# Kernel optimization log

Measured on AMD Instinct MI355X. Metric: run time of the kernel, lower is better.

Reference implementation:

```python
import jax, jax.numpy as jnp
import numpy as np

N = 50000   # nodes
E = 1600000 # edges
G = 512     # graphs in batch
IN_DIM, EMBED, H, D = 64, 128, 4, 32
D1, D2, D3 = 128, 64, 16
NEG_SLOPE = 0.2  # DGL GATConv default


def setup_inputs() -> dict:
    key = jax.random.key(0)
    ks = jax.random.split(key, 16)
    def glorot(k, shape):
        fan = shape[0] + shape[-1]
        return jax.random.normal(k, shape, jnp.float32) * jnp.sqrt(2.0 / fan)
    return {
        "feature": jax.random.normal(ks[0], (N, IN_DIM), jnp.float32),
        "src": jax.random.randint(ks[1], (E,), 0, N, jnp.int32),
        "dst": jax.random.randint(ks[2], (E,), 0, N, jnp.int32),
        "graph_ids": jnp.sort(jax.random.randint(ks[3], (N,), 0, G, jnp.int32)),
        "W0": glorot(ks[4], (IN_DIM, EMBED)), "b0": jnp.zeros((EMBED,), jnp.float32),
        "Wfc": glorot(ks[5], (EMBED, H * D)),
        "attn_l": glorot(ks[6], (H, D)), "attn_r": glorot(ks[7], (H, D)),
        "gat_bias": jnp.zeros((H * D,), jnp.float32),
        "W1": glorot(ks[8], (H * D, D1)), "b1": jnp.zeros((D1,), jnp.float32),
        "W2": glorot(ks[9], (D1, D2)), "b2": jnp.zeros((D2,), jnp.float32),
        "W3": glorot(ks[10], (D2, D3)), "b3": jnp.zeros((D3,), jnp.float32),
    }


def reference(feature, src, dst, graph_ids, W0, b0, Wfc, attn_l, attn_r,
              gat_bias, W1, b1, W2, b2, W3, b3):
    # initial dense embed
    h = feature @ W0 + b0                                   # [N, EMBED]
    # GATConv
    feat = (h @ Wfc).reshape(N, H, D)                       # [N,H,D]
    el = jnp.einsum('nhd,hd->nh', feat, attn_l)             # [N,H]
    er = jnp.einsum('nhd,hd->nh', feat, attn_r)
    e = jax.nn.leaky_relu(el[src] + er[dst], NEG_SLOPE)     # [E,H]
    # segment softmax over incoming edges of each dst node
    m = jax.ops.segment_max(e, dst, num_segments=N)         # [N,H]
    ex = jnp.exp(e - m[dst])                                # [E,H]
    denom = jax.ops.segment_sum(ex, dst, num_segments=N)    # [N,H]
    a = ex / denom[dst]                                     # [E,H]
    msg = a[:, :, None] * feat[src]                         # [E,H,D]
    rst = jax.ops.segment_sum(msg, dst, num_segments=N)     # [N,H,D]
    rst = rst + gat_bias.reshape(1, H, D)
    hn = rst.reshape(N, H * D)
    # AvgPooling per graph
    sums = jax.ops.segment_sum(hn, graph_ids, num_segments=G)           # [G,H*D]
    cnts = jax.ops.segment_sum(jnp.ones((N,), hn.dtype), graph_ids, num_segments=G)
    hg = sums / jnp.maximum(cnts, 1.0)[:, None]
    # dense head
    out = jax.nn.elu(hg)
    out = jax.nn.elu(out @ W1 + b1)
    out = jax.nn.elu(out @ W2 + b2)
    out = out @ W3 + b3                                     # [G, D3]
    atten = a[:, :, None]                                   # [E,H,1] like DGL
    return out, atten
```

## Files before the change

kernel.cpp:

```cpp
#include <hip/hip_runtime.h>
#include <hip/hip_fp16.h>
#include <math.h>

#define N_NODES 50000
#define E_EDGES 1600000
#define G_GRAPHS 512
#define IN_DIM 64
#define EMBED 128
#define HD 128
#define NHEAD 4
#define D1 128
#define D2 64
#define D3 16
#define NEG_SLOPE 0.2f
#define NB ((N_NODES + 127) >> 7)
#define HT_TILE 4096
#define HT_BLOCKS ((E_EDGES + HT_TILE - 1) / HT_TILE)
#define PT_TILE 8192
#define PT_BLOCKS ((E_EDGES + PT_TILE - 1) / PT_TILE)
#define K1_TILES ((N_NODES + 63) / 64)
#define FB_CAP 8192
#define M2_EDGE_BLK ((E_EDGES + 2047) / 2048)

typedef float vfloat4 __attribute__((ext_vector_type(4)));
typedef float vfloat2 __attribute__((ext_vector_type(2)));
typedef unsigned short ushort_t;

static __device__ __forceinline__ float leaky(float x) { return x > 0.f ? x : NEG_SLOPE * x; }

__global__ void __launch_bounds__(256) k0hg(const int* __restrict__ dst, int* __restrict__ ghist,
                                            const float* __restrict__ W0, const float* __restrict__ b0,
                                            const float* __restrict__ Wfc, float* __restrict__ Wc,
                                            float* __restrict__ bc) {
    __shared__ int lh[NB];
    const int t = threadIdx.x;
    if (blockIdx.x < HT_BLOCKS) {
        for (int i = t; i < NB; i += 256) lh[i] = 0;
        __syncthreads();
        const long e0 = (long)blockIdx.x * HT_TILE;
#pragma unroll
        for (int k = 0; k < HT_TILE / 256; ++k) {
            long e = e0 + t + k * 256;
            if (e < E_EDGES) atomicAdd(&lh[dst[e] >> 7], 1);
        }
        __syncthreads();
        for (int i = t; i < NB; i += 256) {
            int v = lh[i];
            if (v) atomicAdd(&ghist[i], v);
        }
    } else {
        int tid = (int)(blockIdx.x - HT_BLOCKS) * 256 + t;
        if (tid < IN_DIM * HD) {
            int i = tid >> 7, j = tid & 127;
            float acc = 0.f;
            for (int k = 0; k < EMBED; ++k) acc += W0[i * EMBED + k] * Wfc[k * HD + j];
            Wc[tid] = acc;
        } else if (tid < IN_DIM * HD + HD) {
            int j = tid - IN_DIM * HD;
            float acc = 0.f;
            for (int k = 0; k < EMBED; ++k) acc += b0[k] * Wfc[k * HD + j];
            bc[j] = acc;
        }
    }
}

#define SMEM_BYTES 53248
__global__ void __launch_bounds__(256) k1pt(
    const float* __restrict__ A, const float* __restrict__ W,
    const float* __restrict__ b, const float* __restrict__ attn_l,
    const float* __restrict__ attn_r,
    const int* __restrict__ src, const int* __restrict__ dst,
    const int* __restrict__ ghist, int* __restrict__ cursor0,
    unsigned char* __restrict__ feat, float* __restrict__ el,
    float* __restrict__ er, unsigned int* __restrict__ part) {
    __shared__ __align__(16) char smem[SMEM_BYTES];
    const int t = threadIdx.x;
    if (blockIdx.x < K1_TILES) {
        float* Ws = (float*)smem;
        float(*As)[68] = (float(*)[68])(smem + 32768);
        const int cc = t & 31, rt = t >> 5;
        const int c0 = cc * 4, r0 = rt * 8;
        const int row0 = (int)blockIdx.x * 64;
        {
            const float4* Wg = (const float4*)W;
            float4* Wl = (float4*)Ws;
#pragma unroll
            for (int j = 0; j < (IN_DIM * HD / 4) / 256; ++j) Wl[t + j * 256] = Wg[t + j * 256];
        }
#pragma unroll
        for (int j = 0; j < 4; ++j) {
            int i2 = t + j * 256;
            int row = i2 >> 4, kq = i2 & 15;
            int gr = row0 + row;
            float4 v = (gr < N_NODES) ? *(const float4*)(A + (size_t)gr * IN_DIM + kq * 4)
                                      : make_float4(0.f, 0.f, 0.f, 0.f);
            *(float4*)&As[row][kq * 4] = v;
        }
        __syncthreads();
        float acc[8][4];
#pragma unroll
        for (int i = 0; i < 8; ++i)
#pragma unroll
            for (int j = 0; j < 4; ++j) acc[i][j] = 0.f;
        for (int k4 = 0; k4 < IN_DIM / 4; ++k4) {
            vfloat4 w0 = *(const vfloat4*)&Ws[(k4 * 4 + 0) * HD + c0];
            vfloat4 w1 = *(const vfloat4*)&Ws[(k4 * 4 + 1) * HD + c0];
            vfloat4 w2 = *(const vfloat4*)&Ws[(k4 * 4 + 2) * HD + c0];
            vfloat4 w3 = *(const vfloat4*)&Ws[(k4 * 4 + 3) * HD + c0];
#pragma unroll
            for (int i = 0; i < 8; ++i) {
                vfloat4 a = *(const vfloat4*)&As[r0 + i][k4 * 4];
#pragma unroll
                for (int j = 0; j < 4; ++j)
                    acc[i][j] += a.x * w0[j] + a.y * w1[j] + a.z * w2[j] + a.w * w3[j];
            }
        }
        {
            vfloat4 bcv = *(const vfloat4*)(b + c0);
#pragma unroll
            for (int i = 0; i < 8; ++i)
#pragma unroll
                for (int j = 0; j < 4; ++j) acc[i][j] += bcv[j];
        }
#pragma unroll
        for (int i = 0; i < 8; ++i) {
            int gr = row0 + r0 + i;
            if (gr < N_NODES) {
                unsigned int ww = __builtin_amdgcn_cvt_pk_fp8_f32(acc[i][0], acc[i][1], 0, false);
                ww = __builtin_amdgcn_cvt_pk_fp8_f32(acc[i][2], acc[i][3], ww, true);
                *(unsigned int*)(feat + (size_t)gr * HD + c0) = ww;
            }
        }
        {
            vfloat4 al = *(const vfloat4*)(attn_l + c0);
            vfloat4 ar = *(const vfloat4*)(attn_r + c0);
            float pl[8], pr[8];
#pragma unroll
            for (int i = 0; i < 8; ++i) {
                pl[i] = acc[i][0] * al[0] + acc[i][1] * al[1] + acc[i][2] * al[2] + acc[i][3] * al[3];
                pr[i] = acc[i][0] * ar[0] + acc[i][1] * ar[1] + acc[i][2] * ar[2] + acc[i][3] * ar[3];
            }
#pragma unroll
            for (int off = 1; off <= 4; off <<= 1) {
#pragma unroll
                for (int i = 0; i < 8; ++i) {
                    pl[i] += __shfl_xor(pl[i], off);
                    pr[i] += __shfl_xor(pr[i], off);
                }
            }
            if ((cc & 7) == 0) {
                const int h = cc >> 3;
#pragma unroll
                for (int i = 0; i < 8; ++i) {
                    int gr = row0 + r0 + i;
                    if (gr < N_NODES) {
                        el[gr * 4 + h] = pl[i];
                        er[gr * 4 + h] = pr[i];
                    }
                }
            }
        }
    } else {
        int(*hist)[NB] = (int(*)[NB])smem;
        int(*lcur)[NB] = (int(*)[NB])(smem + 6256);
        int* tot = (int*)(smem + 12512);
        int* offs = (int*)(smem + 14076);
        int* base_s = (int*)(smem + 15640);
        int* gt = (int*)(smem + 17204);
        int* offsG = (int*)(smem + 18768);
        unsigned int* stage = (unsigned int*)(smem + 20336);
        const int lane = t & 63, wid = t >> 6;
        const int tile = (int)blockIdx.x - K1_TILES;
        const long e0 = (long)tile * PT_TILE;
        const int cnt = (int)min((long)PT_TILE, (long)E_EDGES - e0);
        for (int i = t; i < NB; i += 256) {
            hist[0][i] = 0; hist[1][i] = 0; hist[2][i] = 0; hist[3][i] = 0;
            gt[i] = ghist[i];
        }
        __syncthreads();
        unsigned int v[PT_TILE / 256];
#pragma unroll
        for (int k = 0; k < PT_TILE / 256; ++k) {
            int i = t + k * 256;
            if (i < cnt) {
                int d = dst[e0 + i];
                v[k] = ((unsigned int)d << 16) | (unsigned int)src[e0 + i];
                atomicAdd(&hist[wid][d >> 7], 1);
            } else v[k] = 0xFFFFFFFFu;
        }
        __syncthreads();
        for (int i = t; i < NB; i += 256) {
            int h0 = hist[0][i], h1 = hist[1][i], h2 = hist[2][i], h3 = hist[3][i];
            hist[0][i] = 0; hist[1][i] = h0; hist[2][i] = h0 + h1; hist[3][i] = h0 + h1 + h2;
            tot[i] = h0 + h1 + h2 + h3;
        }
        __syncthreads();
        if (wid == 0) {
            int run = 0;
            for (int c = 0; c < (NB + 63) / 64; ++c) {
                int i = c * 64 + lane;
                int vv = (i < NB) ? tot[i] : 0;
                int incl = vv;
#pragma unroll
                for (int off = 1; off < 64; off <<= 1) {
                    int o = __shfl_up(incl, off, 64);
                    if (lane >= off) incl += o;
                }
                if (i < NB) offs[i] = run + incl - vv;
                run += __shfl(incl, 63, 64);
            }
        } else if (wid == 1) {
            int run = 0;
            for (int c = 0; c < (NB + 63) / 64; ++c) {
                int i = c * 64 + lane;
                int vv = (i < NB) ? gt[i] : 0;
                int incl = vv;
#pragma unroll
                for (int off = 1; off < 64; off <<= 1) {
                    int o = __shfl_up(incl, off, 64);
                    if (lane >= off) incl += o;
                }
                if (i < NB) offsG[i] = run + incl - vv;
                run += __shfl(incl, 63, 64);
            }
        }
        __syncthreads();
        for (int i = t; i < NB; i += 256) {
            int tt2 = tot[i];
            base_s[i] = offsG[i] + (tt2 ? atomicAdd(&cursor0[i], tt2) : 0);
            int ob = offs[i];
            lcur[0][i] = ob + hist[0][i];
            lcur[1][i] = ob + hist[1][i];
            lcur[2][i] = ob + hist[2][i];
            lcur[3][i] = ob + hist[3][i];
        }
        __syncthreads();
#pragma unroll
        for (int k = 0; k < PT_TILE / 256; ++k) {
            if (v[k] != 0xFFFFFFFFu) {
                int bb = v[k] >> 23;
                int pos = atomicAdd(&lcur[wid][bb], 1);
                stage[pos] = v[k];
            }
        }
        __syncthreads();
        for (int i = t; i < cnt; i += 256) {
            unsigned int p = stage[i];
            int bb = p >> 23;
            part[base_s[bb] + (i - offs[bb])] = p & 0x7FFFFFu;
        }
    }
}

__global__ void __launch_bounds__(256) fb_fill(const unsigned int* __restrict__ part,
                                               const int* __restrict__ ghist,
                                               int* __restrict__ rowstart,
                                               ushort_t* __restrict__ csr_src) {
    const int b = blockIdx.x, t = threadIdx.x, lane = t & 63, wid = t >> 6;
    __shared__ int degl[4][128], totl[128], offl[128], curl[4][128];
    __shared__ int red[4], s0s[2];
    __shared__ ushort_t lsrc[FB_CAP];
    {
        int partial = 0;
        for (int i = t; i < b; i += 256) partial += ghist[i];
#pragma unroll
        for (int off = 32; off; off >>= 1) partial += __shfl_xor(partial, off);
        if (lane == 0) red[wid] = partial;
        if (t < 128) { degl[0][t] = 0; degl[1][t] = 0; degl[2][t] = 0; degl[3][t] = 0; }
        __syncthreads();
        if (t == 0) {
            int s0 = red[0] + red[1] + red[2] + red[3];
            s0s[0] = s0;
            s0s[1] = s0 + ghist[b];
        }
        __syncthreads();
    }
    const int s0 = s0s[0], s1 = s0s[1];
    const int cnt = s1 - s0;
    for (int i = t; i < cnt; i += 256) {
        unsigned int p = part[s0 + i];
        atomicAdd(&degl[wid][p >> 16], 1);
    }
    __syncthreads();
    if (t < 128) {
        int d0 = degl[0][t], d1 = degl[1][t], d2 = degl[2][t], d3 = degl[3][t];
        degl[0][t] = 0; degl[1][t] = d0; degl[2][t] = d0 + d1; degl[3][t] = d0 + d1 + d2;
        totl[t] = d0 + d1 + d2 + d3;
    }
    __syncthreads();
    if (wid == 0) {
        int run = 0;
        for (int c = 0; c < 2; ++c) {
            int i = c * 64 + lane;
            int vv = totl[i];
            int incl = vv;
#pragma unroll
            for (int off = 1; off < 64; off <<= 1) {
                int o = __shfl_up(incl, off, 64);
                if (lane >= off) incl += o;
            }
            offl[i] = run + incl - vv;
            run += __shfl(incl, 63, 64);
        }
    }
    __syncthreads();
    if (t < 128) {
        int ob = offl[t];
        curl[0][t] = ob + degl[0][t];
        curl[1][t] = ob + degl[1][t];
        curl[2][t] = ob + degl[2][t];
        curl[3][t] = ob + degl[3][t];
        int node = (b << 7) + t;
        if (node < N_NODES) rowstart[node] = s0 + ob;
    }
    if (b == 0 && t == 0) rowstart[N_NODES] = E_EDGES;
    __syncthreads();
    if (cnt <= FB_CAP) {
        for (int i = t; i < cnt; i += 256) {
            unsigned int p = part[s0 + i];
            int pos = atomicAdd(&curl[wid][p >> 16], 1);
            lsrc[pos] = (ushort_t)(p & 0xFFFFu);
        }
        __syncthreads();
        for (int i = t; i < cnt; i += 256) csr_src[s0 + i] = lsrc[i];
    } else {
        for (int i = t; i < cnt; i += 256) {
            unsigned int p = part[s0 + i];
            int pos = atomicAdd(&curl[wid][p >> 16], 1);
            csr_src[s0 + pos] = (ushort_t)(p & 0xFFFFu);
        }
    }
}

__global__ void __launch_bounds__(256) k6_aggregate(
    const ushort_t* __restrict__ csr_src, const int* __restrict__ rowstart,
    const float* __restrict__ el, const float* __restrict__ er,
    const unsigned char* __restrict__ feat, const float* __restrict__ gat_bias,
    float* __restrict__ er_rd, float* __restrict__ hn) {
    __shared__ uint2 s_pk[4][64][4];
    const int wid = threadIdx.x >> 6;
    const int lane = threadIdx.x & 63;
    const int n = blockIdx.x * 4 + wid;
    if (n >= N_NODES) return;
    const int start = rowstart[n];
    const int end = rowstart[n + 1];
    const int deg = end - start;

    const int e0 = lane >> 2;
    const int h = lane & 3;
    const float erh = er[n * 4 + h];
    float sm = 0.f;
    for (int base = 0; base < deg; base += 16) {
        const int e = base + e0;
        if (e < deg) {
            const int s = csr_src[start + e];
            const float ex = __expf(leaky(el[s * 4 + h] + erh));
            sm += ex;
            if (e < 64)
                s_pk[wid][e][h] = make_uint2((unsigned int)s << 7, __float_as_uint(ex));
        }
    }
#pragma unroll
    for (int off = 4; off <= 32; off <<= 1) sm += __shfl_xor(sm, off);
    const float rd = sm > 0.f ? 1.f / sm : 0.f;
    if (lane < 4) {
        er_rd[(size_t)n * 8 + lane] = erh;
        er_rd[(size_t)n * 8 + 4 + lane] = rd;
    }

    const int g4 = lane >> 4, gl = lane & 15;
    const int h2 = gl >> 2;
    const float rdh = __shfl(rd, h2);
    vfloat2 acc0 = {0.f, 0.f}, acc1 = {0.f, 0.f}, acc2 = {0.f, 0.f}, acc3 = {0.f, 0.f};

    if (deg <= 64) {
        const uint2* pk = &s_pk[wid][0][h2];
        const unsigned char* fg = feat + (gl << 3);
        int idx = g4;
        for (; idx + 4 < deg; idx += 8) {
            const uint2 pA = pk[idx * 4];
            const uint2 pB = pk[(idx + 4) * 4];
            const uint2 wA = *(const uint2*)(fg + pA.x);
            const uint2 wB = *(const uint2*)(fg + pB.x);
            const float exA = __uint_as_float(pA.y);
            const float exB = __uint_as_float(pB.y);
            const vfloat2 eA = {exA, exA}, eB = {exB, exB};
            acc0 += eA * __builtin_amdgcn_cvt_pk_f32_fp8(wA.x, false);
            acc1 += eA * __builtin_amdgcn_cvt_pk_f32_fp8(wA.x, true);
            acc2 += eA * __builtin_amdgcn_cvt_pk_f32_fp8(wA.y, false);
            acc3 += eA * __builtin_amdgcn_cvt_pk_f32_fp8(wA.y, true);
            acc0 += eB * __builtin_amdgcn_cvt_pk_f32_fp8(wB.x, false);
            acc1 += eB * __builtin_amdgcn_cvt_pk_f32_fp8(wB.x, true);
            acc2 += eB * __builtin_amdgcn_cvt_pk_f32_fp8(wB.y, false);
            acc3 += eB * __builtin_amdgcn_cvt_pk_f32_fp8(wB.y, true);
        }
        if (idx < deg) {
            const uint2 p = pk[idx * 4];
            const uint2 w = *(const uint2*)(fg + p.x);
            const float ex = __uint_as_float(p.y);
            const vfloat2 ev = {ex, ex};
            acc0 += ev * __builtin_amdgcn_cvt_pk_f32_fp8(w.x, false);
            acc1 += ev * __builtin_amdgcn_cvt_pk_f32_fp8(w.x, true);
            acc2 += ev * __builtin_amdgcn_cvt_pk_f32_fp8(w.y, false);
            acc3 += ev * __builtin_amdgcn_cvt_pk_f32_fp8(w.y, true);
        }
    } else {
        const float erh2 = __shfl(erh, h2);
        const unsigned char* fg = feat + (gl << 3);
        for (int e = start + g4; e < end; e += 4) {
            const unsigned int s = csr_src[e];
            const float ex = __expf(leaky(el[s * 4 + h2] + erh2));
            const vfloat2 ev = {ex, ex};
            const uint2 w = *(const uint2*)(fg + ((size_t)s << 7));
            acc0 += ev * __builtin_amdgcn_cvt_pk_f32_fp8(w.x, false);
            acc1 += ev * __builtin_amdgcn_cvt_pk_f32_fp8(w.x, true);
            acc2 += ev * __builtin_amdgcn_cvt_pk_f32_fp8(w.y, false);
            acc3 += ev * __builtin_amdgcn_cvt_pk_f32_fp8(w.y, true);
        }
    }
    {
        const vfloat2 rv = {rdh, rdh};
        acc0 *= rv; acc1 *= rv; acc2 *= rv; acc3 *= rv;
    }
#pragma unroll
    for (int off = 16; off <= 32; off <<= 1) {
        acc0.x += __shfl_xor(acc0.x, off);
        acc0.y += __shfl_xor(acc0.y, off);
        acc1.x += __shfl_xor(acc1.x, off);
        acc1.y += __shfl_xor(acc1.y, off);
        acc2.x += __shfl_xor(acc2.x, off);
        acc2.y += __shfl_xor(acc2.y, off);
        acc3.x += __shfl_xor(acc3.x, off);
        acc3.y += __shfl_xor(acc3.y, off);
    }
    if (lane < 16) {
        const float4 b0 = ((const float4*)gat_bias)[gl * 2];
        const float4 b1 = ((const float4*)gat_bias)[gl * 2 + 1];
        float4* hp = (float4*)(hn + (size_t)n * HD + gl * 8);
        hp[0] = make_float4(acc0.x + b0.x, acc0.y + b0.y, acc1.x + b0.z, acc1.y + b0.w);
        hp[1] = make_float4(acc2.x + b1.x, acc2.y + b1.y, acc3.x + b1.z, acc3.y + b1.w);
    }
}

__global__ void __launch_bounds__(512) m2b_mlp_attn(
    const int* __restrict__ src, const int* __restrict__ dst,
    const float* __restrict__ el, const float* __restrict__ er_rd,
    const float* __restrict__ hn, const int* __restrict__ graph_ids,
    const float* __restrict__ W1, const float* __restrict__ b1,
    const float* __restrict__ W2, const float* __restrict__ b2,
    const float* __restrict__ W3, const float* __restrict__ b3,
    float* __restrict__ a_out, float* __restrict__ out) {
    const int t = threadIdx.x;
    if (blockIdx.x < G_GRAPHS) {
        const int g = (int)blockIdx.x;
        const int tt = t & 127, part = t >> 7;
        __shared__ int bounds[2];
        __shared__ double pool[4][128];
        __shared__ double x[128], y[128];
        if (t < 2) {
            const int target = g + t;
            int lo = 0, hi = N_NODES;
            while (lo < hi) {
                int mid = (lo + hi) >> 1;
                if (graph_ids[mid] < target) lo = mid + 1; else hi = mid;
            }
            bounds[t] = lo;
        }
        __syncthreads();
        const int lo = bounds[0], hi = bounds[1];
        double s = 0.0;
        for (int n = lo + part; n < hi; n += 4) s += (double)hn[(size_t)n * HD + tt];
        pool[part][tt] = s;
        __syncthreads();
        if (t < 128) {
            const double cnt = (double)(hi - lo);
            const double sum = pool[0][t] + pool[1][t] + pool[2][t] + pool[3][t];
            const double v = sum / fmax(cnt, 1.0);
            x[t] = v > 0.0 ? v : expm1(v);
        }
        __syncthreads();
        if (t < 128) {
            double acc = (double)b1[t];
            for (int k = 0; k < HD; ++k) acc += x[k] * (double)W1[k * D1 + t];
            y[t] = acc > 0.0 ? acc : expm1(acc);
        }
        __syncthreads();
        if (t < D2) {
            double a2 = (double)b2[t];
            for (int k = 0; k < D1; ++k) a2 += y[k] * (double)W2[k * D2 + t];
            x[t] = a2 > 0.0 ? a2 : expm1(a2);
        }
        __syncthreads();
        if (t < D3) {
            double a3 = (double)b3[t];
            for (int k = 0; k < D2; ++k) a3 += x[k] * (double)W3[k * D3 + t];
            out[g * D3 + t] = (float)a3;
        }
    } else {
        const long base = (long)(blockIdx.x - G_GRAPHS) * 2048 + t;
        bool ok[4];
        int sx[4], dx[4];
#pragma unroll
        for (int k = 0; k < 4; ++k) {
            const long e = base + (long)k * 512;
            ok[k] = e < E_EDGES;
            const long ei = ok[k] ? e : 0;
            sx[k] = src[ei];
            dx[k] = dst[ei];
        }
        float4 el4[4], er4[4], r4[4];
#pragma unroll
        for (int k = 0; k < 4; ++k) {
            el4[k] = *(const float4*)(el + sx[k] * 4);
            er4[k] = *(const float4*)(er_rd + (size_t)dx[k] * 8);
            r4[k] = *(const float4*)(er_rd + (size_t)dx[k] * 8 + 4);
        }
#pragma unroll
        for (int k = 0; k < 4; ++k) {
            if (ok[k]) {
                vfloat4 a;
                a.x = __expf(leaky(el4[k].x + er4[k].x)) * r4[k].x;
                a.y = __expf(leaky(el4[k].y + er4[k].y)) * r4[k].y;
                a.z = __expf(leaky(el4[k].z + er4[k].z)) * r4[k].z;
                a.w = __expf(leaky(el4[k].w + er4[k].w)) * r4[k].w;
                __builtin_nontemporal_store(a, (vfloat4*)a_out + (base + (long)k * 512));
            }
        }
    }
}

extern "C" void kernel_launch(void* const* d_in, const int* in_sizes, int n_in,
                              void* d_out, int out_size, void* d_ws, size_t ws_size,
                              hipStream_t stream) {
    const float* feature = (const float*)d_in[0];
    const int* src = (const int*)d_in[1];
    const int* dst = (const int*)d_in[2];
    const int* graph_ids = (const int*)d_in[3];
    const float* W0 = (const float*)d_in[4];
    const float* b0 = (const float*)d_in[5];
    const float* Wfc = (const float*)d_in[6];
    const float* attn_l = (const float*)d_in[7];
    const float* attn_r = (const float*)d_in[8];
    const float* gat_bias = (const float*)d_in[9];
    const float* W1 = (const float*)d_in[10];
    const float* b1 = (const float*)d_in[11];
    const float* W2 = (const float*)d_in[12];
    const float* b2 = (const float*)d_in[13];
    const float* W3 = (const float*)d_in[14];
    const float* b3 = (const float*)d_in[15];

    char* ws = (char*)d_ws;
    size_t off = 0;
    auto carve = [&](size_t bytes) -> void* {
        void* p = ws + off;
        off += (bytes + 255) & ~(size_t)255;
        return p;
    };
    int* ghist = (int*)carve((size_t)NB * 4);
    int* cursor0 = (int*)carve((size_t)NB * 4);
    const size_t zero_span = off;
    float* Wc = (float*)carve((size_t)IN_DIM * HD * 4);
    float* bc = (float*)carve((size_t)HD * 4);
    unsigned char* feat = (unsigned char*)carve((size_t)N_NODES * HD);
    float* el = (float*)carve((size_t)N_NODES * 4 * 4);
    float* er = (float*)carve((size_t)N_NODES * 4 * 4);
    float* er_rd = (float*)carve((size_t)N_NODES * 8 * 4);
    int* rowstart = (int*)carve((size_t)(N_NODES + 1) * 4);
    unsigned int* part = (unsigned int*)carve((size_t)E_EDGES * 4);
    ushort_t* csr_src = (ushort_t*)carve((size_t)E_EDGES * 2);
    float* hn = (float*)carve((size_t)N_NODES * HD * 4);

    float* out = (float*)d_out;
    float* a_out = out + G_GRAPHS * D3;

    (void)hipMemsetAsync(d_ws, 0, zero_span, stream);
    k0hg<<<HT_BLOCKS + 33, 256, 0, stream>>>(dst, ghist, W0, b0, Wfc, Wc, bc);
    k1pt<<<K1_TILES + PT_BLOCKS, 256, 0, stream>>>(feature, Wc, bc, attn_l, attn_r,
                                                   src, dst, ghist, cursor0,
                                                   feat, el, er, part);
    fb_fill<<<NB, 256, 0, stream>>>(part, ghist, rowstart, csr_src);
    k6_aggregate<<<(N_NODES + 3) / 4, 256, 0, stream>>>(csr_src, rowstart, el, er, feat,
                                                        gat_bias, er_rd, hn);
    m2b_mlp_attn<<<G_GRAPHS + M2_EDGE_BLK, 512, 0, stream>>>(src, dst, el, er_rd, hn,
                                                             graph_ids, W1, b1, W2, b2,
                                                             W3, b3, a_out, out);
}
```

Before: 227.6 us.

## Privatize histogram per wave, cache partition in LDS, vectorize edge loads, split aggregate launch

The dst histogram now keeps a separate LDS copy per wavefront to reduce atomic contention. fb_fill caches its partition slice in shared memory so the second pass does not re-read global memory. The attention-output edge loop reads src/dst as int4 for contiguous edges per thread instead of strided scalar loads. k6_aggregate is split into two launches over node halves, which only adds launch overhead with no clear benefit; the extra 32KB of LDS in fb_fill may also lower occupancy.

Measured after the change: 244.5 us. 1.07x slower.

```diff
diff --git a/kernel.cpp b/kernel.cpp
--- a/kernel.cpp
+++ b/kernel.cpp
@@ -21,6 +21,7 @@
 #define K1_TILES ((N_NODES + 63) / 64)
 #define FB_CAP 8192
 #define M2_EDGE_BLK ((E_EDGES + 2047) / 2048)
+#define K6_HALF 6250
 
 typedef float vfloat4 __attribute__((ext_vector_type(4)));
 typedef float vfloat2 __attribute__((ext_vector_type(2)));
@@ -32,20 +33,23 @@
                                             const float* __restrict__ W0, const float* __restrict__ b0,
                                             const float* __restrict__ Wfc, float* __restrict__ Wc,
                                             float* __restrict__ bc) {
-    __shared__ int lh[NB];
+    __shared__ int lh[4][NB];
     const int t = threadIdx.x;
     if (blockIdx.x < HT_BLOCKS) {
-        for (int i = t; i < NB; i += 256) lh[i] = 0;
+        const int wid = t >> 6;
+        for (int i = t; i < NB; i += 256) {
+            lh[0][i] = 0; lh[1][i] = 0; lh[2][i] = 0; lh[3][i] = 0;
+        }
         __syncthreads();
         const long e0 = (long)blockIdx.x * HT_TILE;
 #pragma unroll
         for (int k = 0; k < HT_TILE / 256; ++k) {
             long e = e0 + t + k * 256;
-            if (e < E_EDGES) atomicAdd(&lh[dst[e] >> 7], 1);
+            if (e < E_EDGES) atomicAdd(&lh[wid][dst[e] >> 7], 1);
         }
         __syncthreads();
         for (int i = t; i < NB; i += 256) {
-            int v = lh[i];
+            int v = lh[0][i] + lh[1][i] + lh[2][i] + lh[3][i];
             if (v) atomicAdd(&ghist[i], v);
         }
     } else {
@@ -259,6 +263,7 @@
     const int b = blockIdx.x, t = threadIdx.x, lane = t & 63, wid = t >> 6;
     __shared__ int degl[4][128], totl[128], offl[128], curl[4][128];
     __shared__ int red[4], s0s[2];
+    __shared__ unsigned int lpart[FB_CAP];
     __shared__ ushort_t lsrc[FB_CAP];
     {
         int partial = 0;
@@ -277,9 +282,17 @@
     }
     const int s0 = s0s[0], s1 = s0s[1];
     const int cnt = s1 - s0;
-    for (int i = t; i < cnt; i += 256) {
-        unsigned int p = part[s0 + i];
-        atomicAdd(&degl[wid][p >> 16], 1);
+    if (cnt <= FB_CAP) {
+        for (int i = t; i < cnt; i += 256) {
+            unsigned int p = part[s0 + i];
+            lpart[i] = p;
+            atomicAdd(&degl[wid][p >> 16], 1);
+        }
+    } else {
+        for (int i = t; i < cnt; i += 256) {
+            unsigned int p = part[s0 + i];
+            atomicAdd(&degl[wid][p >> 16], 1);
+        }
     }
     __syncthreads();
     if (t < 128) {
@@ -317,7 +330,7 @@
     __syncthreads();
     if (cnt <= FB_CAP) {
         for (int i = t; i < cnt; i += 256) {
-            unsigned int p = part[s0 + i];
+            unsigned int p = lpart[i];
             int pos = atomicAdd(&curl[wid][p >> 16], 1);
             lsrc[pos] = (ushort_t)(p & 0xFFFFu);
         }
@@ -336,11 +349,11 @@
     const ushort_t* __restrict__ csr_src, const int* __restrict__ rowstart,
     const float* __restrict__ el, const float* __restrict__ er,
     const unsigned char* __restrict__ feat, const float* __restrict__ gat_bias,
-    float* __restrict__ er_rd, float* __restrict__ hn) {
+    float* __restrict__ er_rd, float* __restrict__ hn, int node_base) {
     __shared__ uint2 s_pk[4][64][4];
     const int wid = threadIdx.x >> 6;
     const int lane = threadIdx.x & 63;
-    const int n = blockIdx.x * 4 + wid;
+    const int n = node_base + blockIdx.x * 4 + wid;
     if (n >= N_NODES) return;
     const int start = rowstart[n];
     const int end = rowstart[n + 1];
@@ -497,33 +510,43 @@
             out[g * D3 + t] = (float)a3;
         }
     } else {
-        const long base = (long)(blockIdx.x - G_GRAPHS) * 2048 + t;
-        bool ok[4];
-        int sx[4], dx[4];
-#pragma unroll
-        for (int k = 0; k < 4; ++k) {
-            const long e = base + (long)k * 512;
-            ok[k] = e < E_EDGES;
-            const long ei = ok[k] ? e : 0;
-            sx[k] = src[ei];
-            dx[k] = dst[ei];
-        }
-        float4 el4[4], er4[4], r4[4];
-#pragma unroll
-        for (int k = 0; k < 4; ++k) {
-            el4[k] = *(const float4*)(el + sx[k] * 4);
-            er4[k] = *(const float4*)(er_rd + (size_t)dx[k] * 8);
-            r4[k] = *(const float4*)(er_rd + (size_t)dx[k] * 8 + 4);
-        }
-#pragma unroll
-        for (int k = 0; k < 4; ++k) {
-            if (ok[k]) {
+        const long base4 = (long)(blockIdx.x - G_GRAPHS) * 2048 + (long)t * 4;
+        if (base4 + 3 < E_EDGES) {
+            const int4 s4 = *(const int4*)(src + base4);
+            const int4 d4 = *(const int4*)(dst + base4);
+            const int sx[4] = {s4.x, s4.y, s4.z, s4.w};
+            const int dx[4] = {d4.x, d4.y, d4.z, d4.w};
+            float4 el4[4], er4[4], r4[4];
+#pragma unroll
+            for (int k = 0; k < 4; ++k) {
+                el4[k] = *(const float4*)(el + sx[k] * 4);
+                er4[k] = *(const float4*)(er_rd + (size_t)dx[k] * 8);
+                r4[k] = *(const float4*)(er_rd + (size_t)dx[k] * 8 + 4);
+            }
+#pragma unroll
+            for (int k = 0; k < 4; ++k) {
                 vfloat4 a;
                 a.x = __expf(leaky(el4[k].x + er4[k].x)) * r4[k].x;
                 a.y = __expf(leaky(el4[k].y + er4[k].y)) * r4[k].y;
                 a.z = __expf(leaky(el4[k].z + er4[k].z)) * r4[k].z;
                 a.w = __expf(leaky(el4[k].w + er4[k].w)) * r4[k].w;
-                __builtin_nontemporal_store(a, (vfloat4*)a_out + (base + (long)k * 512));
+                __builtin_nontemporal_store(a, (vfloat4*)a_out + (base4 + k));
+            }
+        } else {
+            for (int k = 0; k < 4; ++k) {
+                const long e = base4 + k;
+                if (e < E_EDGES) {
+                    const int s = src[e], d = dst[e];
+                    const float4 el4 = *(const float4*)(el + s * 4);
+                    const float4 er4 = *(const float4*)(er_rd + (size_t)d * 8);
+                    const float4 r4 = *(const float4*)(er_rd + (size_t)d * 8 + 4);
+                    vfloat4 a;
+                    a.x = __expf(leaky(el4.x + er4.x)) * r4.x;
+                    a.y = __expf(leaky(el4.y + er4.y)) * r4.y;
+                    a.z = __expf(leaky(el4.z + er4.z)) * r4.z;
+                    a.w = __expf(leaky(el4.w + er4.w)) * r4.w;
+                    __builtin_nontemporal_store(a, (vfloat4*)a_out + e);
+                }
             }
         }
     }
@@ -579,8 +602,10 @@
                                                    src, dst, ghist, cursor0,
                                                    feat, el, er, part);
     fb_fill<<<NB, 256, 0, stream>>>(part, ghist, rowstart, csr_src);
-    k6_aggregate<<<(N_NODES + 3) / 4, 256, 0, stream>>>(csr_src, rowstart, el, er, feat,
-                                                        gat_bias, er_rd, hn);
+    k6_aggregate<<<K6_HALF, 256, 0, stream>>>(csr_src, rowstart, el, er, feat,
+                                              gat_bias, er_rd, hn, 0);
+    k6_aggregate<<<K6_HALF, 256, 0, stream>>>(csr_src, rowstart, el, er, feat,
+                                              gat_bias, er_rd, hn, 25000);
     m2b_mlp_attn<<<G_GRAPHS + M2_EDGE_BLK, 512, 0, stream>>>(src, dst, el, er_rd, hn,
                                                              graph_ids, W1, b1, W2, b2,
                                                              W3, b3, a_out, out);
```
